# Kernel optimization log

Hardware: AMD Instinct MI355X
Metric: run time of the kernel (lower is better)

The kernel has to match this reference:

```python
import jax, jax.numpy as jnp
import numpy as np

N = 50000
E = 800000
F_IN = 500
H = 5          # heads
C = 32         # per-head channels
HID = H * C    # 160
NC = 20        # num_classes
G = 8          # number of graphs in batch
SLOPE_ATT = 0.2   # GATConv attention leaky slope (PyG default)
SLOPE_ACT = 0.01  # F.leaky_relu default


def _layernorm(x, scale, bias, eps=1e-5):
    mu = jnp.mean(x, axis=-1, keepdims=True)
    var = jnp.var(x, axis=-1, keepdims=True)
    return (x - mu) * jax.lax.rsqrt(var + eps) * scale + bias


def _edge_softmax(logits, dst, num_nodes):
    # segment softmax over incoming edges of each destination node
    m = jax.ops.segment_max(logits, dst, num_segments=num_nodes)
    ex = jnp.exp(logits - m[dst])
    s = jax.ops.segment_sum(ex, dst, num_segments=num_nodes)
    return ex / (s[dst] + 1e-16)


def _gat_layer(x, src, dst, W, a_src, a_dst, b):
    n = x.shape[0]
    h = (x @ W).reshape(n, H, C)                       # [N,H,C]
    al_s = jnp.einsum('nhc,hc->nh', h, a_src)          # [N,H]
    al_d = jnp.einsum('nhc,hc->nh', h, a_dst)
    logits = jax.nn.leaky_relu(al_s[src] + al_d[dst], SLOPE_ATT)  # [Et,H]
    alpha = _edge_softmax(logits, dst, n)              # [Et,H]
    msg = h[src] * alpha[..., None]                    # [Et,H,C]
    out = jax.ops.segment_sum(msg, dst, num_segments=n).reshape(n, HID) + b
    return out, alpha


def setup_inputs():
    key = jax.random.key(0)
    ks = jax.random.split(key, 24)
    p = lambda k, shp: jax.random.normal(k, shp, jnp.float32) * 0.05
    x = jax.random.normal(ks[0], (N, F_IN), jnp.float32)
    edge_index = jax.random.randint(ks[1], (2, E), 0, N, jnp.int64)
    batch = jnp.sort(jax.random.randint(ks[2], (N,), 0, G, jnp.int64))
    return {
        'x': x, 'edge_index': edge_index, 'batch': batch,
        'W1': p(ks[3], (F_IN, HID)), 'a_src1': p(ks[4], (H, C)), 'a_dst1': p(ks[5], (H, C)), 'b1': jnp.zeros((HID,), jnp.float32),
        'ln1_s': jnp.ones((HID,), jnp.float32), 'ln1_b': jnp.zeros((HID,), jnp.float32),
        'W2': p(ks[6], (HID, HID)), 'a_src2': p(ks[7], (H, C)), 'a_dst2': p(ks[8], (H, C)), 'b2': jnp.zeros((HID,), jnp.float32),
        'ln2_s': jnp.ones((HID,), jnp.float32), 'ln2_b': jnp.zeros((HID,), jnp.float32),
        'Wm': p(ks[9], (HID, HID)), 'bm': jnp.zeros((HID,), jnp.float32),
        'Wmlp1': p(ks[10], (HID, HID)), 'bmlp1': jnp.zeros((HID,), jnp.float32),
        'ln3_s': jnp.ones((HID,), jnp.float32), 'ln3_b': jnp.zeros((HID,), jnp.float32),
        'Wmlp2': p(ks[11], (HID, NC)), 'bmlp2': jnp.zeros((NC,), jnp.float32),
    }


def reference(x, edge_index, batch, W1, a_src1, a_dst1, b1, ln1_s, ln1_b,
              W2, a_src2, a_dst2, b2, ln2_s, ln2_b, Wm, bm,
              Wmlp1, bmlp1, ln3_s, ln3_b, Wmlp2, bmlp2):
    n = x.shape[0]
    # PyG GATConv adds self-loops by default
    loops = jnp.arange(n, dtype=edge_index.dtype)
    src = jnp.concatenate([edge_index[0], loops])
    dst = jnp.concatenate([edge_index[1], loops])

    h1, alpha1 = _gat_layer(x, src, dst, W1, a_src1, a_dst1, b1)
    h1 = jax.nn.leaky_relu(h1, SLOPE_ACT)
    h1 = _layernorm(h1, ln1_s, ln1_b)      # dropout = identity at eval

    h2, alpha2 = _gat_layer(h1, src, dst, W2, a_src2, a_dst2, b2)
    h2 = jax.nn.leaky_relu(h2, SLOPE_ACT)
    h2 = _layernorm(h2, ln2_s, ln2_b)

    xo = jax.nn.leaky_relu(h2 @ Wm + bm, SLOPE_ACT)   # [N,HID]

    # global_mean_pool over batch assignment
    sums = jax.ops.segment_sum(xo, batch, num_segments=G)
    cnts = jax.ops.segment_sum(jnp.ones((n, 1), xo.dtype), batch, num_segments=G)
    pooled = sums / jnp.maximum(cnts, 1.0)            # [G,HID]

    z = pooled @ Wmlp1 + bmlp1
    z = jax.nn.relu(_layernorm(z, ln3_s, ln3_b))
    rec = z @ Wmlp2 + bmlp2                           # [G,NC]
    return xo, rec, alpha1, alpha2
```

## Files before the change

### kernel.cpp

```cpp
#include <hip/hip_runtime.h>
#include <hip/hip_bf16.h>
#include <cstdint>
#include <cstddef>

#define NN   50000
#define EE   800000
#define ET_  (EE + NN)
#define FIN  500
#define HID_ 160
#define NC_  20
#define GG   8
#define GB1  ((NN + 63) / 64)
#define NK1  16
#define NK2  5
#define EBH  ((ET_ + 255) / 256)

typedef __attribute__((ext_vector_type(8))) short ab8;
typedef __attribute__((ext_vector_type(4))) float f4;

static __device__ __forceinline__ unsigned short f2bf(float v) {
    union { float f; uint32_t u; } c; c.f = v;
    uint32_t r = c.u + 0x7FFFu + ((c.u >> 16) & 1u);
    return (unsigned short)(r >> 16);
}

static __device__ __forceinline__ float2 bf2f2(uint32_t u) {
    union { uint32_t u; float f; } a, b;
    a.u = u << 16;
    b.u = u & 0xffff0000u;
    return make_float2(a.f, b.f);
}

static __device__ __forceinline__ int lbound_i(const int* arr, int n, int val) {
    int lo = 0, hi = n;
    while (lo < hi) { int mid = (lo + hi) >> 1; if (arr[mid] < val) lo = mid + 1; else hi = mid; }
    return lo;
}

__global__ __launch_bounds__(256) void k_prep0(const float* __restrict__ W1, ab8* __restrict__ B1,
                                               const float* __restrict__ W2, ab8* __restrict__ B2,
                                               const float* __restrict__ Wm, ab8* __restrict__ Bm,
                                               float* __restrict__ pooled, int* __restrict__ deg) {
    int idx = blockIdx.x * 256 + threadIdx.x;
    if (idx < NN) deg[idx] = 0;
    if (idx < GG * HID_) pooled[idx] = 0.f;
    const int C1 = NK1 * 10 * 64;
    const int C2 = NK2 * 10 * 64;
    const float* W; ab8* Bo; int K, cidx;
    if (idx < C1)                { W = W1; Bo = B1; K = FIN;  cidx = idx; }
    else if (idx < C1 + C2)      { W = W2; Bo = B2; K = HID_; cidx = idx - C1; }
    else if (idx < C1 + 2 * C2)  { W = Wm; Bo = Bm; K = HID_; cidx = idx - C1 - C2; }
    else return;
    int s = cidx / 640, r = cidx % 640;
    int t = r >> 6, l = r & 63;
    int fr = l & 15, q = l >> 4;
    int n  = t * 16 + fr;
    int k0 = s * 32 + q * 8;
    unsigned short pk[8];
#pragma unroll
    for (int j = 0; j < 8; j++) {
        int k = k0 + j;
        pk[j] = (k < K) ? f2bf(W[(size_t)k * HID_ + n]) : (unsigned short)0;
    }
    Bo[cidx] = *reinterpret_cast<ab8*>(pk);
}

__global__ __launch_bounds__(256) void k_hist_conv(const int* __restrict__ ei, int* __restrict__ deg,
                                                   const float* __restrict__ x, ab8* __restrict__ Apk) {
    if (blockIdx.x >= GB1) {
        int e = (blockIdx.x - GB1) * 256 + threadIdx.x;
        if (e >= ET_) return;
        int d = (e < EE) ? ei[EE + e] : (e - EE);
        atomicAdd(&deg[d], 1);
        return;
    }
    __shared__ uint2 lds2[4096];
    int blk = blockIdx.x;
    int tid = threadIdx.x;
    const float4* xf4 = (const float4*)x;
    uint4* ap4 = (uint4*)Apk;
#pragma unroll
    for (int h = 0; h < 2; h++) {
        for (int i = tid; i < 4096; i += 256) lds2[i] = make_uint2(0u, 0u);
        __syncthreads();
        int rbase = blk * 64 + h * 32;
        for (int i = tid; i < 4000; i += 256) {
            int rl = i / 125, j = i - rl * 125;
            int g = rbase + rl;
            if (g < NN) {
                float4 v = xf4[(size_t)g * 125 + j];
                uint32_t lo = (uint32_t)f2bf(v.x) | ((uint32_t)f2bf(v.y) << 16);
                uint32_t hi = (uint32_t)f2bf(v.z) | ((uint32_t)f2bf(v.w) << 16);
                int k = j * 4;
                int s = k >> 5, q = (k >> 3) & 3, e2 = (k & 7) >> 2;
                int woff = rl >> 4, fr = rl & 15;
                int idx = s * 128 + woff * 64 + q * 16 + fr;
                int p = idx ^ (((s << 2) | q) & 7);
                lds2[2 * p + e2] = make_uint2(lo, hi);
            }
        }
        __syncthreads();
        for (int i = tid; i < 2048; i += 256) {
            int s = i >> 7, off = i & 127;
            int q = (off >> 4) & 3;
            int p = i ^ (((s << 2) | q) & 7);
            uint2 a = lds2[2 * p], b = lds2[2 * p + 1];
            ap4[(size_t)(blk * NK1 + s) * 256 + h * 128 + off] = make_uint4(a.x, a.y, b.x, b.y);
        }
        __syncthreads();
    }
}

__global__ __launch_bounds__(256) void k_scan1(const int* __restrict__ deg, int* __restrict__ rowptr,
                                               int* __restrict__ bsum) {
    __shared__ int s[256];
    int t = threadIdx.x;
    int base = blockIdx.x * 1024 + t * 4;
    int v0 = (base + 0 < NN) ? deg[base + 0] : 0;
    int v1 = (base + 1 < NN) ? deg[base + 1] : 0;
    int v2 = (base + 2 < NN) ? deg[base + 2] : 0;
    int v3 = (base + 3 < NN) ? deg[base + 3] : 0;
    int tot = v0 + v1 + v2 + v3;
    s[t] = tot;
    __syncthreads();
    for (int off = 1; off < 256; off <<= 1) {
        int y = (t >= off) ? s[t - off] : 0;
        __syncthreads();
        s[t] += y;
        __syncthreads();
    }
    int excl = s[t] - tot;
    if (t == 255) bsum[blockIdx.x] = s[255];
    if (base + 0 < NN) rowptr[base + 0] = excl;  excl += v0;
    if (base + 1 < NN) rowptr[base + 1] = excl;  excl += v1;
    if (base + 2 < NN) rowptr[base + 2] = excl;  excl += v2;
    if (base + 3 < NN) rowptr[base + 3] = excl;
}

__global__ void k_scan2(int* __restrict__ bsum, int nb) {
    int t = threadIdx.x;
    int v = (t < nb) ? bsum[t] : 0;
    int orig = v;
    for (int off = 1; off < 64; off <<= 1) {
        int y = __shfl_up(v, off);
        if (t >= off) v += y;
    }
    if (t < nb) bsum[t] = v - orig;
}

__global__ __launch_bounds__(256) void k_scan3(int* __restrict__ rowptr, const int* __restrict__ bsum,
                                               int* __restrict__ cursor) {
    int i = blockIdx.x * 256 + threadIdx.x;
    if (i < NN) {
        int r = rowptr[i] + bsum[i >> 10];
        rowptr[i] = r;
        cursor[i] = r;
    }
    if (i == NN) rowptr[NN] = ET_;
}

static __device__ __forceinline__ void gemm_body(int blk,
                                                 const ab8* __restrict__ Apk,
                                                 const ab8* __restrict__ Bpk, int nk,
                                                 float* __restrict__ C, __hip_bfloat16* __restrict__ Cb,
                                                 int M,
                                                 const float* __restrict__ bias, int act,
                                                 const float* __restrict__ asrc, const float* __restrict__ adst,
                                                 float* __restrict__ als_o, float* __restrict__ ald_o,
                                                 const int* __restrict__ batch_p, float* __restrict__ pooled) {
    int tid  = threadIdx.x;
    int lane = tid & 63;
    int w    = tid >> 6;
    int fr   = lane & 15;
    int q    = lane >> 4;
    int row0 = blk * 64;

    f4 acc[10];
#pragma unroll
    for (int t = 0; t < 10; t++) acc[t] = (f4)0.f;

    const ab8* bb  = Bpk + lane;
    const ab8* apk = Apk + (size_t)blk * nk * 256 + tid;

    ab8 bcur[10], bnx[10];
#pragma unroll
    for (int t = 0; t < 10; t++) bcur[t] = bb[t * 64];
    ab8 a0 = apk[0];
    ab8 a1 = apk[256];
    for (int s = 0; s < nk; s++) {
        if (s + 1 < nk) {
#pragma unroll
            for (int t = 0; t < 10; t++) bnx[t] = bb[((s + 1) * 10 + t) * 64];
        }
        ab8 a2 = (ab8)0;
        if (s + 2 < nk) a2 = apk[(s + 2) * 256];
#pragma unroll
        for (int t = 0; t < 10; t++)
            acc[t] = __builtin_amdgcn_mfma_f32_16x16x32_bf16(a0, bcur[t], acc[t], 0, 0, 0);
        a0 = a1; a1 = a2;
#pragma unroll
        for (int t = 0; t < 10; t++) bcur[t] = bnx[t];
    }

    if (als_o) {
        float av_s[10], av_d[10];
#pragma unroll
        for (int t = 0; t < 10; t++) { av_s[t] = asrc[t * 16 + fr]; av_d[t] = adst[t * 16 + fr]; }
#pragma unroll
        for (int i = 0; i < 4; i++) {
            int r = row0 + w * 16 + q * 4 + i;
            float ps[5], pd[5];
#pragma unroll
            for (int h = 0; h < 5; h++) {
                ps[h] = acc[2 * h][i] * av_s[2 * h] + acc[2 * h + 1][i] * av_s[2 * h + 1];
                pd[h] = acc[2 * h][i] * av_d[2 * h] + acc[2 * h + 1][i] * av_d[2 * h + 1];
            }
#pragma unroll
            for (int off = 8; off >= 1; off >>= 1)
#pragma unroll
                for (int h = 0; h < 5; h++) {
                    ps[h] += __shfl_xor(ps[h], off);
                    pd[h] += __shfl_xor(pd[h], off);
                }
            if (fr == 0 && r < M) {
#pragma unroll
                for (int h = 0; h < 5; h++) {
                    als_o[(size_t)r * 8 + h] = ps[h];
                    ald_o[(size_t)r * 8 + h] = pd[h];
                }
            }
        }
    }

    int gu = -2;
    if (pooled) {
        int rhi = row0 + 63; if (rhi >= M) rhi = M - 1;
        int gl = batch_p[row0], gh = batch_p[rhi];
        gu = (gl == gh) ? gl : -1;
    }
    float psum[10];
#pragma unroll
    for (int t = 0; t < 10; t++) psum[t] = 0.f;

    int rbase = row0 + w * 16 + q * 4;
#pragma unroll
    for (int t = 0; t < 10; t++) {
        int col = t * 16 + fr;
        float bv = bias ? bias[col] : 0.f;
#pragma unroll
        for (int i = 0; i < 4; i++) {
            int r = rbase + i;
            float v = acc[t][i] + bv;
            if (act) v = v > 0.f ? v : 0.01f * v;
            if (r < M) {
                if (C)  C[(size_t)r * HID_ + col] = v;
                if (Cb) *reinterpret_cast<unsigned short*>(&Cb[(size_t)r * HID_ + col]) = f2bf(v);
                if (gu >= 0) psum[t] += v;
                else if (gu == -1) atomicAdd(&pooled[batch_p[r] * HID_ + col], v);
            }
        }
    }
    if (gu >= 0) {
#pragma unroll
        for (int t = 0; t < 10; t++) {
            psum[t] += __shfl_xor(psum[t], 16);
            psum[t] += __shfl_xor(psum[t], 32);
        }
        if (q == 0) {
#pragma unroll
            for (int t = 0; t < 10; t++)
                atomicAdd(&pooled[gu * HID_ + t * 16 + fr], psum[t]);
        }
    }
}

__global__ __launch_bounds__(256) void k_gemm_scatter(const ab8* __restrict__ Apk,
                                                      const ab8* __restrict__ Bpk, int nk,
                                                      float* __restrict__ C, __hip_bfloat16* __restrict__ Cb,
                                                      int M,
                                                      const float* __restrict__ bias, int act,
                                                      const float* __restrict__ asrc, const float* __restrict__ adst,
                                                      float* __restrict__ als_o, float* __restrict__ ald_o,
                                                      const int* __restrict__ batch_p, float* __restrict__ pooled,
                                                      const int* __restrict__ ei, int* __restrict__ cursor,
                                                      int* __restrict__ esrc) {
    if (blockIdx.x < GB1) {
        gemm_body(blockIdx.x, Apk, Bpk, nk, C, Cb, M, bias, act, asrc, adst, als_o, ald_o, batch_p, pooled);
    } else {
        int e = (blockIdx.x - GB1) * 256 + threadIdx.x;
        if (e >= ET_) return;
        int s, d;
        if (e < EE) { s = ei[e]; d = ei[EE + e]; } else { s = e - EE; d = e - EE; }
        int slot = atomicAdd(&cursor[d], 1);
        esrc[slot] = s;
    }
}

static __device__ __forceinline__ void alpha_body(int e, const int* __restrict__ ei,
                                                  const float* __restrict__ als, const float* __restrict__ ald,
                                                  const float* __restrict__ invb,
                                                  float* __restrict__ alpha_out) {
    if (e >= ET_) return;
    int s, d;
    if (e < EE) { s = ei[e]; d = ei[EE + e]; } else { s = e - EE; d = e - EE; }
    const float* as = &als[(size_t)s * 8];
    float4 a4 = *reinterpret_cast<const float4*>(as);
    float  a5 = as[4];
    float asv[5] = {a4.x, a4.y, a4.z, a4.w, a5};
    const float* adp = &ald[(size_t)d * 8];
    float4 d4 = *reinterpret_cast<const float4*>(adp);
    float  d5 = adp[4];
    float adv[5] = {d4.x, d4.y, d4.z, d4.w, d5};
    const float* ip = &invb[(size_t)d * 8];
    float4 i4 = *reinterpret_cast<const float4*>(ip);
    float  i5 = ip[4];
    float ivv[5] = {i4.x, i4.y, i4.z, i4.w, i5};
    float* ao = &alpha_out[(size_t)e * 5];
#pragma unroll
    for (int h = 0; h < 5; h++) {
        float l = asv[h] + adv[h];
        l = l > 0.f ? l : 0.2f * l;
        float ex = __expf(fminf(l, 60.f));
        ao[h] = ex * ivv[h];
    }
}

__global__ __launch_bounds__(256) void k_gemm_alpha(const ab8* __restrict__ Apk,
                                                    const ab8* __restrict__ Bpk, int nk,
                                                    float* __restrict__ C, __hip_bfloat16* __restrict__ Cb,
                                                    int M,
                                                    const float* __restrict__ bias, int act,
                                                    const float* __restrict__ asrc, const float* __restrict__ adst,
                                                    float* __restrict__ als_o, float* __restrict__ ald_o,
                                                    const int* __restrict__ batch_p, float* __restrict__ pooled,
                                                    const int* __restrict__ ei,
                                                    const float* __restrict__ als_r, const float* __restrict__ ald_r,
                                                    const float* __restrict__ invb, float* __restrict__ alpha_out) {
    if (blockIdx.x < GB1) {
        gemm_body(blockIdx.x, Apk, Bpk, nk, C, Cb, M, bias, act, asrc, adst, als_o, ald_o, batch_p, pooled);
    } else {
        int e = (blockIdx.x - GB1) * 256 + threadIdx.x;
        alpha_body(e, ei, als_r, ald_r, invb, alpha_out);
    }
}

__global__ __launch_bounds__(256) void k_att_agg(const int* __restrict__ rowptr,
                                                 const int* __restrict__ esrc,
                                                 const float* __restrict__ als, const float* __restrict__ ald,
                                                 const __hip_bfloat16* __restrict__ hmat,
                                                 float* __restrict__ alphap,
                                                 float* __restrict__ invb,
                                                 const float* __restrict__ bias,
                                                 const float* __restrict__ lns, const float* __restrict__ lnb,
                                                 uint4* __restrict__ xpk) {
    __shared__ float sExp[4][64 * 5];
    __shared__ int   sSrc[4][64];
    int wv   = threadIdx.x >> 6;
    int lane = threadIdx.x & 63;
    int node = blockIdx.x * 4 + wv;
    if (node >= NN) return;
    int start = rowptr[node], end = rowptr[node + 1];
    int deg = end - start;
    bool fits = (deg <= 64);
    float4 dd4 = *reinterpret_cast<const float4*>(&ald[(size_t)node * 8]);
    float  dd5 = ald[(size_t)node * 8 + 4];
    float ad[5] = {dd4.x, dd4.y, dd4.z, dd4.w, dd5};

    float sm[5] = {0.f, 0.f, 0.f, 0.f, 0.f};
    for (int j = start + lane; j < end; j += 64) {
        int sy = esrc[j];
        int idx = j - start;
        if (fits) sSrc[wv][idx] = sy;
        const float* as = &als[(size_t)sy * 8];
        float4 a4 = *reinterpret_cast<const float4*>(as);
        float  a5 = as[4];
        float asv[5] = {a4.x, a4.y, a4.z, a4.w, a5};
#pragma unroll
        for (int h = 0; h < 5; h++) {
            float l = asv[h] + ad[h];
            l = l > 0.f ? l : 0.2f * l;
            float ex = __expf(fminf(l, 60.f));
            sm[h] += ex;
            if (fits) sExp[wv][idx * 5 + h] = ex;
            else      alphap[(size_t)j * 5 + h] = ex;
        }
    }
#pragma unroll
    for (int off = 32; off >= 1; off >>= 1)
#pragma unroll
        for (int h = 0; h < 5; h++) sm[h] += __shfl_xor(sm[h], off);
    float inv[5];
#pragma unroll
    for (int h = 0; h < 5; h++) inv[h] = 1.f / (sm[h] + 1e-16f);
    if (lane == 0) {
        float* ip = &invb[(size_t)node * 8];
        ip[0] = inv[0]; ip[1] = inv[1]; ip[2] = inv[2]; ip[3] = inv[3]; ip[4] = inv[4];
    }
    if (fits && lane < deg) {
#pragma unroll
        for (int h = 0; h < 5; h++) sExp[wv][lane * 5 + h] *= inv[h];
    }

    int h0 = lane >> 4;
    bool lo16 = lane < 16;
    int c01 = 2 * lane;
    int c2  = 128 + 2 * lane;
    float2 A0 = make_float2(0.f, 0.f), A1 = make_float2(0.f, 0.f);
    float2 A2 = make_float2(0.f, 0.f), A3 = make_float2(0.f, 0.f);
    float2 H0 = make_float2(0.f, 0.f), H1 = make_float2(0.f, 0.f);
    float2 H2 = make_float2(0.f, 0.f), H3 = make_float2(0.f, 0.f);

    if (fits) {
        int idx = 0;
        for (; idx + 3 < deg; idx += 4) {
            int s0 = sSrc[wv][idx], s1 = sSrc[wv][idx + 1];
            int s2 = sSrc[wv][idx + 2], s3 = sSrc[wv][idx + 3];
            float w0 = sExp[wv][(idx + 0) * 5 + h0];
            float w1 = sExp[wv][(idx + 1) * 5 + h0];
            float w2 = sExp[wv][(idx + 2) * 5 + h0];
            float w3 = sExp[wv][(idx + 3) * 5 + h0];
            const unsigned short* r0 = (const unsigned short*)&hmat[(size_t)s0 * HID_];
            const unsigned short* r1 = (const unsigned short*)&hmat[(size_t)s1 * HID_];
            const unsigned short* r2 = (const unsigned short*)&hmat[(size_t)s2 * HID_];
            const unsigned short* r3 = (const unsigned short*)&hmat[(size_t)s3 * HID_];
            float2 f0 = bf2f2(*reinterpret_cast<const uint32_t*>(&r0[c01]));
            float2 f1 = bf2f2(*reinterpret_cast<const uint32_t*>(&r1[c01]));
            float2 f2 = bf2f2(*reinterpret_cast<const uint32_t*>(&r2[c01]));
            float2 f3 = bf2f2(*reinterpret_cast<const uint32_t*>(&r3[c01]));
            A0.x += w0 * f0.x; A0.y += w0 * f0.y;
            A1.x += w1 * f1.x; A1.y += w1 * f1.y;
            A2.x += w2 * f2.x; A2.y += w2 * f2.y;
            A3.x += w3 * f3.x; A3.y += w3 * f3.y;
            if (lo16) {
                float u0 = sExp[wv][(idx + 0) * 5 + 4];
                float u1 = sExp[wv][(idx + 1) * 5 + 4];
                float u2 = sExp[wv][(idx + 2) * 5 + 4];
                float u3 = sExp[wv][(idx + 3) * 5 + 4];
                float2 g0 = bf2f2(*reinterpret_cast<const uint32_t*>(&r0[c2]));
                float2 g1 = bf2f2(*reinterpret_cast<const uint32_t*>(&r1[c2]));
                float2 g2 = bf2f2(*reinterpret_cast<const uint32_t*>(&r2[c2]));
                float2 g3 = bf2f2(*reinterpret_cast<const uint32_t*>(&r3[c2]));
                H0.x += u0 * g0.x; H0.y += u0 * g0.y;
                H1.x += u1 * g1.x; H1.y += u1 * g1.y;
                H2.x += u2 * g2.x; H2.y += u2 * g2.y;
                H3.x += u3 * g3.x; H3.y += u3 * g3.y;
            }
        }
        for (; idx < deg; idx++) {
            int s0 = sSrc[wv][idx];
            float w0 = sExp[wv][idx * 5 + h0];
            const unsigned short* r0 = (const unsigned short*)&hmat[(size_t)s0 * HID_];
            float2 f0 = bf2f2(*reinterpret_cast<const uint32_t*>(&r0[c01]));
            A0.x += w0 * f0.x; A0.y += w0 * f0.y;
            if (lo16) {
                float u0 = sExp[wv][idx * 5 + 4];
                float2 g0 = bf2f2(*reinterpret_cast<const uint32_t*>(&r0[c2]));
                H0.x += u0 * g0.x; H0.y += u0 * g0.y;
            }
        }
    } else {
        for (int j = start; j < end; j++) {
            int s0 = esrc[j];
            float w0 = alphap[(size_t)j * 5 + h0] * inv[h0];
            const unsigned short* r0 = (const unsigned short*)&hmat[(size_t)s0 * HID_];
            float2 f0 = bf2f2(*reinterpret_cast<const uint32_t*>(&r0[c01]));
            A0.x += w0 * f0.x; A0.y += w0 * f0.y;
            if (lo16) {
                float u0 = alphap[(size_t)j * 5 + 4] * inv[4];
                float2 g0 = bf2f2(*reinterpret_cast<const uint32_t*>(&r0[c2]));
                H0.x += u0 * g0.x; H0.y += u0 * g0.y;
            }
        }
    }
    float2 A = make_float2(A0.x + A1.x + A2.x + A3.x, A0.y + A1.y + A2.y + A3.y);
    float2 Hh = make_float2(H0.x + H1.x + H2.x + H3.x, H0.y + H1.y + H2.y + H3.y);

    float2 bb = *reinterpret_cast<const float2*>(&bias[c01]);
    float v0 = A.x + bb.x;  v0 = v0 > 0.f ? v0 : 0.01f * v0;
    float v1 = A.y + bb.y;  v1 = v1 > 0.f ? v1 : 0.01f * v1;
    float v2 = 0.f, v3 = 0.f;
    if (lo16) {
        float2 b2 = *reinterpret_cast<const float2*>(&bias[c2]);
        v2 = Hh.x + b2.x; v2 = v2 > 0.f ? v2 : 0.01f * v2;
        v3 = Hh.y + b2.y; v3 = v3 > 0.f ? v3 : 0.01f * v3;
    }
    float s  = v0 + v1 + v2 + v3;
    float sq = v0 * v0 + v1 * v1 + v2 * v2 + v3 * v3;
#pragma unroll
    for (int off = 32; off >= 1; off >>= 1) {
        s  += __shfl_xor(s, off);
        sq += __shfl_xor(sq, off);
    }
    float m = s * (1.f / 160.f);
    float r = rsqrtf(sq * (1.f / 160.f) - m * m + 1e-5f);
    uint32_t pk1, pk2 = 0u;
    {
        float2 sc = *reinterpret_cast<const float2*>(&lns[c01]);
        float2 bi = *reinterpret_cast<const float2*>(&lnb[c01]);
        pk1 = (uint32_t)f2bf((v0 - m) * r * sc.x + bi.x)
            | ((uint32_t)f2bf((v1 - m) * r * sc.y + bi.y) << 16);
    }
    if (lo16) {
        float2 sc = *reinterpret_cast<const float2*>(&lns[c2]);
        float2 bi = *reinterpret_cast<const float2*>(&lnb[c2]);
        pk2 = (uint32_t)f2bf((v2 - m) * r * sc.x + bi.x)
            | ((uint32_t)f2bf((v3 - m) * r * sc.y + bi.y) << 16);
    }
    int j = lane;
    int srcb = (j < 16) ? (4 * j) : (4 * ((j - 16) & 15));
    uint32_t a0w = __shfl(pk1, srcb + 0), a1w = __shfl(pk1, srcb + 1);
    uint32_t a2w = __shfl(pk1, srcb + 2), a3w = __shfl(pk1, srcb + 3);
    uint32_t b0w = __shfl(pk2, srcb + 0), b1w = __shfl(pk2, srcb + 1);
    uint32_t b2w = __shfl(pk2, srcb + 2), b3w = __shfl(pk2, srcb + 3);
    if (j < 20) {
        uint4 val;
        val.x = (j < 16) ? a0w : b0w;
        val.y = (j < 16) ? a1w : b1w;
        val.z = (j < 16) ? a2w : b2w;
        val.w = (j < 16) ? a3w : b3w;
        int blk = node >> 6, wq = (node >> 4) & 3, fr = node & 15;
        int ks = j >> 2, q = j & 3;
        size_t cidx = (size_t)(blk * NK2 + ks) * 256 + wq * 64 + q * 16 + fr;
        xpk[cidx] = val;
    }
}

__global__ __launch_bounds__(256) void k_mlp(const float* __restrict__ pooled, const int* __restrict__ batch,
                                             const float* __restrict__ W1, const float* __restrict__ b1,
                                             const float* __restrict__ lns, const float* __restrict__ lnb,
                                             const float* __restrict__ W2, const float* __restrict__ b2,
                                             float* __restrict__ rec) {
    __shared__ float P[GG][HID_];
    __shared__ float Z[GG][HID_];
    __shared__ float mu[GG], rr[GG], ic[GG];
    int t = threadIdx.x;
    if (t < GG) {
        int lo = lbound_i(batch, NN, t), hi = lbound_i(batch, NN, t + 1);
        ic[t] = 1.f / fmaxf((float)(hi - lo), 1.f);
    }
    __syncthreads();
    for (int i = t; i < GG * HID_; i += 256) P[i / HID_][i % HID_] = pooled[i] * ic[i / HID_];
    __syncthreads();
    for (int i = t; i < GG * HID_; i += 256) {
        int g = i / HID_, j = i % HID_;
        float acc = b1[j];
        for (int k = 0; k < HID_; k++) acc += P[g][k] * W1[k * HID_ + j];
        Z[g][j] = acc;
    }
    __syncthreads();
    if (t < GG) {
        float s = 0.f, sq = 0.f;
        for (int k = 0; k < HID_; k++) { float z = Z[t][k]; s += z; sq += z * z; }
        float m = s / (float)HID_;
        mu[t] = m;
        rr[t] = rsqrtf(sq / (float)HID_ - m * m + 1e-5f);
    }
    __syncthreads();
    for (int i = t; i < GG * HID_; i += 256) {
        int g = i / HID_, j = i % HID_;
        float z = (Z[g][j] - mu[g]) * rr[g] * lns[j] + lnb[j];
        Z[g][j] = fmaxf(z, 0.f);
    }
    __syncthreads();
    for (int i = t; i < GG * NC_; i += 256) {
        int g = i / NC_, j = i % NC_;
        float acc = b2[j];
        for (int k = 0; k < HID_; k++) acc += Z[g][k] * W2[k * NC_ + j];
        rec[g * NC_ + j] = acc;
    }
}

extern "C" void kernel_launch(void* const* d_in, const int* in_sizes, int n_in,
                              void* d_out, int out_size, void* d_ws, size_t ws_size,
                              hipStream_t stream) {
    const float* x    = (const float*)d_in[0];
    const int*   ei   = (const int*)d_in[1];
    const int*   batch= (const int*)d_in[2];
    const float* W1   = (const float*)d_in[3];
    const float* as1  = (const float*)d_in[4];
    const float* ad1  = (const float*)d_in[5];
    const float* b1   = (const float*)d_in[6];
    const float* ln1s = (const float*)d_in[7];
    const float* ln1b = (const float*)d_in[8];
    const float* W2   = (const float*)d_in[9];
    const float* as2  = (const float*)d_in[10];
    const float* ad2  = (const float*)d_in[11];
    const float* b2   = (const float*)d_in[12];
    const float* ln2s = (const float*)d_in[13];
    const float* ln2b = (const float*)d_in[14];
    const float* Wm   = (const float*)d_in[15];
    const float* bm   = (const float*)d_in[16];
    const float* Wm1  = (const float*)d_in[17];
    const float* bm1  = (const float*)d_in[18];
    const float* ln3s = (const float*)d_in[19];
    const float* ln3b = (const float*)d_in[20];
    const float* Wm2  = (const float*)d_in[21];
    const float* bm2  = (const float*)d_in[22];

    float* out    = (float*)d_out;
    float* xo     = out;
    float* rec    = out + (size_t)NN * HID_;
    float* alpha1 = rec + GG * NC_;
    float* alpha2 = alpha1 + (size_t)ET_ * 5;

    char* w = (char*)d_ws;
    auto carve = [&](size_t bytes) { char* p = w; w += (bytes + 255) & ~(size_t)255; return p; };
    int*   deg    = (int*)carve((size_t)NN * 4);
    int*   rowptr = (int*)carve((size_t)(NN + 1) * 4);
    int*   cursor = (int*)carve((size_t)NN * 4);
    int*   esrc   = (int*)carve((size_t)ET_ * 4);
    int*   bsum   = (int*)carve(64 * 4);
    __hip_bfloat16* hbuf = (__hip_bfloat16*)carve((size_t)NN * HID_ * 2);
    uint4* xpk    = (uint4*)carve((size_t)GB1 * NK2 * 256 * 16);
    float* alphap = (float*)carve((size_t)ET_ * 5 * 4);
    float* als1   = (float*)carve((size_t)NN * 8 * 4);
    float* ald1   = (float*)carve((size_t)NN * 8 * 4);
    float* als2   = (float*)carve((size_t)NN * 8 * 4);
    float* ald2   = (float*)carve((size_t)NN * 8 * 4);
    float* invb   = (float*)carve((size_t)NN * 8 * 4);
    float* pooled = (float*)carve((size_t)GG * HID_ * 4);
    ab8*   B1pk   = (ab8*)carve((size_t)NK1 * 10 * 64 * 16);
    ab8*   B2pk   = (ab8*)carve((size_t)NK2 * 10 * 64 * 16);
    ab8*   Bmpk   = (ab8*)carve((size_t)NK2 * 10 * 64 * 16);
    ab8*   Apk    = (ab8*)d_out;

    k_prep0<<<(NN + 255) / 256, 256, 0, stream>>>(W1, B1pk, W2, B2pk, Wm, Bmpk, pooled, deg);

    k_hist_conv<<<GB1 + EBH, 256, 0, stream>>>(ei, deg, x, Apk);

    int nb = (NN + 1023) / 1024;
    k_scan1<<<nb, 256, 0, stream>>>(deg, rowptr, bsum);
    k_scan2<<<1, 64, 0, stream>>>(bsum, nb);
    k_scan3<<<(NN + 1 + 255) / 256, 256, 0, stream>>>(rowptr, bsum, cursor);

    const int NWB = (NN + 3) / 4;

    k_gemm_scatter<<<GB1 + EBH, 256, 0, stream>>>(Apk, B1pk, NK1, nullptr, hbuf, NN, nullptr, 0,
                                                  as1, ad1, als1, ald1, nullptr, nullptr,
                                                  ei, cursor, esrc);

    k_att_agg<<<NWB, 256, 0, stream>>>(rowptr, esrc, als1, ald1, hbuf, alphap, invb,
                                       b1, ln1s, ln1b, xpk);

    k_gemm_alpha<<<GB1 + EBH, 256, 0, stream>>>((const ab8*)xpk, B2pk, NK2, nullptr, hbuf, NN,
                                                nullptr, 0, as2, ad2, als2, ald2, nullptr, nullptr,
                                                ei, als1, ald1, invb, alpha1);

    k_att_agg<<<NWB, 256, 0, stream>>>(rowptr, esrc, als2, ald2, hbuf, alphap, invb,
                                       b2, ln2s, ln2b, xpk);

    k_gemm_alpha<<<GB1 + EBH, 256, 0, stream>>>((const ab8*)xpk, Bmpk, NK2, xo, nullptr, NN,
                                                bm, 1, nullptr, nullptr, nullptr, nullptr, batch, pooled,
                                                ei, als2, ald2, invb, alpha2);

    k_mlp<<<1, 256, 0, stream>>>(pooled, batch, Wm1, bm1, ln3s, ln3b, Wm2, bm2, rec);
}
```

Measured before the change: 600.2 us.

## Fuse x bf16 conversion into first GEMM via LDS staging, merge prep with histogram

Removes the separate pass that converted x to packed bf16 in global memory. The first-layer GEMM now loads fp32 x directly, converts and swizzles it into LDS in two halves, then runs MFMA from LDS. This avoids writing and re-reading about 50 MB of packed A. Weight packing is merged into the degree histogram kernel, and deg is zeroed with a memset. The cost is extra syncthreads and LDS traffic inside the GEMM, and the conversion work now sits on the GEMM's critical path.

Measured after the change: 613.5 us. 1.02x slower.

```diff
diff --git a/kernel.cpp b/kernel.cpp
--- a/kernel.cpp
+++ b/kernel.cpp
@@ -14,6 +14,7 @@
 #define NK1  16
 #define NK2  5
 #define EBH  ((ET_ + 255) / 256)
+#define PREPB ((NK1 * 10 * 64 + 2 * NK2 * 10 * 64 + 255) / 256)
 
 typedef __attribute__((ext_vector_type(8))) short ab8;
 typedef __attribute__((ext_vector_type(4))) float f4;
@@ -37,12 +38,19 @@
     return lo;
 }
 
-__global__ __launch_bounds__(256) void k_prep0(const float* __restrict__ W1, ab8* __restrict__ B1,
-                                               const float* __restrict__ W2, ab8* __restrict__ B2,
-                                               const float* __restrict__ Wm, ab8* __restrict__ Bm,
-                                               float* __restrict__ pooled, int* __restrict__ deg) {
-    int idx = blockIdx.x * 256 + threadIdx.x;
-    if (idx < NN) deg[idx] = 0;
+__global__ __launch_bounds__(256) void k_prep_hist(const float* __restrict__ W1, ab8* __restrict__ B1,
+                                                   const float* __restrict__ W2, ab8* __restrict__ B2,
+                                                   const float* __restrict__ Wm, ab8* __restrict__ Bm,
+                                                   float* __restrict__ pooled,
+                                                   const int* __restrict__ ei, int* __restrict__ deg) {
+    if (blockIdx.x < EBH) {
+        int e = blockIdx.x * 256 + threadIdx.x;
+        if (e >= ET_) return;
+        int d = (e < EE) ? ei[EE + e] : (e - EE);
+        atomicAdd(&deg[d], 1);
+        return;
+    }
+    int idx = (blockIdx.x - EBH) * 256 + threadIdx.x;
     if (idx < GG * HID_) pooled[idx] = 0.f;
     const int C1 = NK1 * 10 * 64;
     const int C2 = NK2 * 10 * 64;
@@ -63,52 +71,6 @@
         pk[j] = (k < K) ? f2bf(W[(size_t)k * HID_ + n]) : (unsigned short)0;
     }
     Bo[cidx] = *reinterpret_cast<ab8*>(pk);
-}
-
-__global__ __launch_bounds__(256) void k_hist_conv(const int* __restrict__ ei, int* __restrict__ deg,
-                                                   const float* __restrict__ x, ab8* __restrict__ Apk) {
-    if (blockIdx.x >= GB1) {
-        int e = (blockIdx.x - GB1) * 256 + threadIdx.x;
-        if (e >= ET_) return;
-        int d = (e < EE) ? ei[EE + e] : (e - EE);
-        atomicAdd(&deg[d], 1);
-        return;
-    }
-    __shared__ uint2 lds2[4096];
-    int blk = blockIdx.x;
-    int tid = threadIdx.x;
-    const float4* xf4 = (const float4*)x;
-    uint4* ap4 = (uint4*)Apk;
-#pragma unroll
-    for (int h = 0; h < 2; h++) {
-        for (int i = tid; i < 4096; i += 256) lds2[i] = make_uint2(0u, 0u);
-        __syncthreads();
-        int rbase = blk * 64 + h * 32;
-        for (int i = tid; i < 4000; i += 256) {
-            int rl = i / 125, j = i - rl * 125;
-            int g = rbase + rl;
-            if (g < NN) {
-                float4 v = xf4[(size_t)g * 125 + j];
-                uint32_t lo = (uint32_t)f2bf(v.x) | ((uint32_t)f2bf(v.y) << 16);
-                uint32_t hi = (uint32_t)f2bf(v.z) | ((uint32_t)f2bf(v.w) << 16);
-                int k = j * 4;
-                int s = k >> 5, q = (k >> 3) & 3, e2 = (k & 7) >> 2;
-                int woff = rl >> 4, fr = rl & 15;
-                int idx = s * 128 + woff * 64 + q * 16 + fr;
-                int p = idx ^ (((s << 2) | q) & 7);
-                lds2[2 * p + e2] = make_uint2(lo, hi);
-            }
-        }
-        __syncthreads();
-        for (int i = tid; i < 2048; i += 256) {
-            int s = i >> 7, off = i & 127;
-            int q = (off >> 4) & 3;
-            int p = i ^ (((s << 2) | q) & 7);
-            uint2 a = lds2[2 * p], b = lds2[2 * p + 1];
-            ap4[(size_t)(blk * NK1 + s) * 256 + h * 128 + off] = make_uint4(a.x, a.y, b.x, b.y);
-        }
-        __syncthreads();
-    }
 }
 
 __global__ __launch_bounds__(256) void k_scan1(const int* __restrict__ deg, int* __restrict__ rowptr,
@@ -159,6 +121,89 @@
     if (i == NN) rowptr[NN] = ET_;
 }
 
+static __device__ __forceinline__ void gemm_epilogue(f4 (&acc)[10], int row0, int M,
+                                                     float* __restrict__ C, __hip_bfloat16* __restrict__ Cb,
+                                                     const float* __restrict__ bias, int act,
+                                                     const float* __restrict__ asrc, const float* __restrict__ adst,
+                                                     float* __restrict__ als_o, float* __restrict__ ald_o,
+                                                     const int* __restrict__ batch_p, float* __restrict__ pooled) {
+    int lane = threadIdx.x & 63;
+    int w    = threadIdx.x >> 6;
+    int fr   = lane & 15;
+    int q    = lane >> 4;
+
+    if (als_o) {
+        float av_s[10], av_d[10];
+#pragma unroll
+        for (int t = 0; t < 10; t++) { av_s[t] = asrc[t * 16 + fr]; av_d[t] = adst[t * 16 + fr]; }
+#pragma unroll
+        for (int i = 0; i < 4; i++) {
+            int r = row0 + w * 16 + q * 4 + i;
+            float ps[5], pd[5];
+#pragma unroll
+            for (int h = 0; h < 5; h++) {
+                ps[h] = acc[2 * h][i] * av_s[2 * h] + acc[2 * h + 1][i] * av_s[2 * h + 1];
+                pd[h] = acc[2 * h][i] * av_d[2 * h] + acc[2 * h + 1][i] * av_d[2 * h + 1];
+            }
+#pragma unroll
+            for (int off = 8; off >= 1; off >>= 1)
+#pragma unroll
+                for (int h = 0; h < 5; h++) {
+                    ps[h] += __shfl_xor(ps[h], off);
+                    pd[h] += __shfl_xor(pd[h], off);
+                }
+            if (fr == 0 && r < M) {
+#pragma unroll
+                for (int h = 0; h < 5; h++) {
+                    als_o[(size_t)r * 8 + h] = ps[h];
+                    ald_o[(size_t)r * 8 + h] = pd[h];
+                }
+            }
+        }
+    }
+
+    int gu = -2;
+    if (pooled) {
+        int rhi = row0 + 63; if (rhi >= M) rhi = M - 1;
+        int gl = batch_p[row0], gh = batch_p[rhi];
+        gu = (gl == gh) ? gl : -1;
+    }
+    float psum[10];
+#pragma unroll
+    for (int t = 0; t < 10; t++) psum[t] = 0.f;
+
+    int rbase = row0 + w * 16 + q * 4;
+#pragma unroll
+    for (int t = 0; t < 10; t++) {
+        int col = t * 16 + fr;
+        float bv = bias ? bias[col] : 0.f;
+#pragma unroll
+        for (int i = 0; i < 4; i++) {
+            int r = rbase + i;
+            float v = acc[t][i] + bv;
+            if (act) v = v > 0.f ? v : 0.01f * v;
+            if (r < M) {
+                if (C)  C[(size_t)r * HID_ + col] = v;
+                if (Cb) *reinterpret_cast<unsigned short*>(&Cb[(size_t)r * HID_ + col]) = f2bf(v);
+                if (gu >= 0) psum[t] += v;
+                else if (gu == -1) atomicAdd(&pooled[batch_p[r] * HID_ + col], v);
+            }
+        }
+    }
+    if (gu >= 0) {
+#pragma unroll
+        for (int t = 0; t < 10; t++) {
+            psum[t] += __shfl_xor(psum[t], 16);
+            psum[t] += __shfl_xor(psum[t], 32);
+        }
+        if (q == 0) {
+#pragma unroll
+            for (int t = 0; t < 10; t++)
+                atomicAdd(&pooled[gu * HID_ + t * 16 + fr], psum[t]);
+        }
+    }
+}
+
 static __device__ __forceinline__ void gemm_body(int blk,
                                                  const ab8* __restrict__ Apk,
                                                  const ab8* __restrict__ Bpk, int nk,
@@ -170,9 +215,6 @@
                                                  const int* __restrict__ batch_p, float* __restrict__ pooled) {
     int tid  = threadIdx.x;
     int lane = tid & 63;
-    int w    = tid >> 6;
-    int fr   = lane & 15;
-    int q    = lane >> 4;
     int row0 = blk * 64;
 
     f4 acc[10];
@@ -201,99 +243,81 @@
 #pragma unroll
         for (int t = 0; t < 10; t++) bcur[t] = bnx[t];
     }
-
-    if (als_o) {
-        float av_s[10], av_d[10];
-#pragma unroll
-        for (int t = 0; t < 10; t++) { av_s[t] = asrc[t * 16 + fr]; av_d[t] = adst[t * 16 + fr]; }
-#pragma unroll
-        for (int i = 0; i < 4; i++) {
-            int r = row0 + w * 16 + q * 4 + i;
-            float ps[5], pd[5];
-#pragma unroll
-            for (int h = 0; h < 5; h++) {
-                ps[h] = acc[2 * h][i] * av_s[2 * h] + acc[2 * h + 1][i] * av_s[2 * h + 1];
-                pd[h] = acc[2 * h][i] * av_d[2 * h] + acc[2 * h + 1][i] * av_d[2 * h + 1];
-            }
-#pragma unroll
-            for (int off = 8; off >= 1; off >>= 1)
-#pragma unroll
-                for (int h = 0; h < 5; h++) {
-                    ps[h] += __shfl_xor(ps[h], off);
-                    pd[h] += __shfl_xor(pd[h], off);
-                }
-            if (fr == 0 && r < M) {
-#pragma unroll
-                for (int h = 0; h < 5; h++) {
-                    als_o[(size_t)r * 8 + h] = ps[h];
-                    ald_o[(size_t)r * 8 + h] = pd[h];
-                }
-            }
-        }
-    }
-
-    int gu = -2;
-    if (pooled) {
-        int rhi = row0 + 63; if (rhi >= M) rhi = M - 1;
-        int gl = batch_p[row0], gh = batch_p[rhi];
-        gu = (gl == gh) ? gl : -1;
-    }
-    float psum[10];
-#pragma unroll
-    for (int t = 0; t < 10; t++) psum[t] = 0.f;
-
-    int rbase = row0 + w * 16 + q * 4;
-#pragma unroll
-    for (int t = 0; t < 10; t++) {
-        int col = t * 16 + fr;
-        float bv = bias ? bias[col] : 0.f;
-#pragma unroll
-        for (int i = 0; i < 4; i++) {
-            int r = rbase + i;
-            float v = acc[t][i] + bv;
-            if (act) v = v > 0.f ? v : 0.01f * v;
-            if (r < M) {
-                if (C)  C[(size_t)r * HID_ + col] = v;
-                if (Cb) *reinterpret_cast<unsigned short*>(&Cb[(size_t)r * HID_ + col]) = f2bf(v);
-                if (gu >= 0) psum[t] += v;
-                else if (gu == -1) atomicAdd(&pooled[batch_p[r] * HID_ + col], v);
-            }
-        }
-    }
-    if (gu >= 0) {
-#pragma unroll
-        for (int t = 0; t < 10; t++) {
-            psum[t] += __shfl_xor(psum[t], 16);
-            psum[t] += __shfl_xor(psum[t], 32);
-        }
-        if (q == 0) {
-#pragma unroll
-            for (int t = 0; t < 10; t++)
-                atomicAdd(&pooled[gu * HID_ + t * 16 + fr], psum[t]);
-        }
-    }
-}
-
-__global__ __launch_bounds__(256) void k_gemm_scatter(const ab8* __restrict__ Apk,
-                                                      const ab8* __restrict__ Bpk, int nk,
-                                                      float* __restrict__ C, __hip_bfloat16* __restrict__ Cb,
-                                                      int M,
-                                                      const float* __restrict__ bias, int act,
-                                                      const float* __restrict__ asrc, const float* __restrict__ adst,
-                                                      float* __restrict__ als_o, float* __restrict__ ald_o,
-                                                      const int* __restrict__ batch_p, float* __restrict__ pooled,
-                                                      const int* __restrict__ ei, int* __restrict__ cursor,
-                                                      int* __restrict__ esrc) {
-    if (blockIdx.x < GB1) {
-        gemm_body(blockIdx.x, Apk, Bpk, nk, C, Cb, M, bias, act, asrc, adst, als_o, ald_o, batch_p, pooled);
-    } else {
+    gemm_epilogue(acc, row0, M, C, Cb, bias, act, asrc, adst, als_o, ald_o, batch_p, pooled);
+}
+
+__global__ __launch_bounds__(256) void k_gemm1_scatter(const float* __restrict__ x,
+                                                       const ab8* __restrict__ Bpk,
+                                                       __hip_bfloat16* __restrict__ Cb, int M,
+                                                       const float* __restrict__ asrc, const float* __restrict__ adst,
+                                                       float* __restrict__ als_o, float* __restrict__ ald_o,
+                                                       const int* __restrict__ ei, int* __restrict__ cursor,
+                                                       int* __restrict__ esrc) {
+    if (blockIdx.x >= GB1) {
         int e = (blockIdx.x - GB1) * 256 + threadIdx.x;
         if (e >= ET_) return;
         int s, d;
         if (e < EE) { s = ei[e]; d = ei[EE + e]; } else { s = e - EE; d = e - EE; }
         int slot = atomicAdd(&cursor[d], 1);
         esrc[slot] = s;
-    }
+        return;
+    }
+    __shared__ __align__(16) uint2 lds2[4096];
+    int blk  = blockIdx.x;
+    int tid  = threadIdx.x;
+    int lane = tid & 63;
+    int q    = lane >> 4;
+    int row0 = blk * 64;
+
+    f4 acc[10];
+#pragma unroll
+    for (int t = 0; t < 10; t++) acc[t] = (f4)0.f;
+
+    const ab8* bb = Bpk + lane;
+    ab8 bcur[10], bnx[10];
+#pragma unroll
+    for (int t = 0; t < 10; t++) bcur[t] = bb[t * 64];
+
+    const float4* xf4 = (const float4*)x;
+
+#pragma unroll
+    for (int half = 0; half < 2; half++) {
+        for (int i = tid; i < 4096; i += 256) lds2[i] = make_uint2(0u, 0u);
+        __syncthreads();
+        for (int i = tid; i < 4096; i += 256) {
+            int rl = i >> 6, j = i & 63;
+            int fidx = half * 64 + j;
+            int g = row0 + rl;
+            if (g < M && fidx < 125) {
+                float4 v = xf4[(size_t)g * 125 + fidx];
+                uint32_t lo = (uint32_t)f2bf(v.x) | ((uint32_t)f2bf(v.y) << 16);
+                uint32_t hi = (uint32_t)f2bf(v.z) | ((uint32_t)f2bf(v.w) << 16);
+                int sl = j >> 3, qq = (j >> 1) & 3, e2 = j & 1;
+                int chunk = sl * 256 + (rl >> 4) * 64 + qq * 16 + (rl & 15);
+                int p = chunk ^ (((sl << 2) | qq) & 7);
+                lds2[2 * p + e2] = make_uint2(lo, hi);
+            }
+        }
+        __syncthreads();
+        for (int sl = 0; sl < 8; sl++) {
+            int s = half * 8 + sl;
+            if (s + 1 < NK1) {
+#pragma unroll
+                for (int t = 0; t < 10; t++) bnx[t] = bb[((s + 1) * 10 + t) * 64];
+            }
+            int chunk = sl * 256 + tid;
+            int p = chunk ^ (((sl << 2) | q) & 7);
+            uint4 av = *reinterpret_cast<uint4*>(&lds2[2 * p]);
+            ab8 a0 = *reinterpret_cast<ab8*>(&av);
+#pragma unroll
+            for (int t = 0; t < 10; t++)
+                acc[t] = __builtin_amdgcn_mfma_f32_16x16x32_bf16(a0, bcur[t], acc[t], 0, 0, 0);
+#pragma unroll
+            for (int t = 0; t < 10; t++) bcur[t] = bnx[t];
+        }
+        __syncthreads();
+    }
+    gemm_epilogue(acc, row0, M, nullptr, Cb, nullptr, 0, asrc, adst, als_o, ald_o, nullptr, nullptr);
 }
 
 static __device__ __forceinline__ void alpha_body(int e, const int* __restrict__ ei,
@@ -622,11 +646,10 @@
     ab8*   B1pk   = (ab8*)carve((size_t)NK1 * 10 * 64 * 16);
     ab8*   B2pk   = (ab8*)carve((size_t)NK2 * 10 * 64 * 16);
     ab8*   Bmpk   = (ab8*)carve((size_t)NK2 * 10 * 64 * 16);
-    ab8*   Apk    = (ab8*)d_out;
-
-    k_prep0<<<(NN + 255) / 256, 256, 0, stream>>>(W1, B1pk, W2, B2pk, Wm, Bmpk, pooled, deg);
-
-    k_hist_conv<<<GB1 + EBH, 256, 0, stream>>>(ei, deg, x, Apk);
+
+    hipMemsetAsync(deg, 0, (size_t)NN * 4, stream);
+
+    k_prep_hist<<<EBH + PREPB, 256, 0, stream>>>(W1, B1pk, W2, B2pk, Wm, Bmpk, pooled, ei, deg);
 
     int nb = (NN + 1023) / 1024;
     k_scan1<<<nb, 256, 0, stream>>>(deg, rowptr, bsum);
@@ -635,9 +658,8 @@
 
     const int NWB = (NN + 3) / 4;
 
-    k_gemm_scatter<<<GB1 + EBH, 256, 0, stream>>>(Apk, B1pk, NK1, nullptr, hbuf, NN, nullptr, 0,
-                                                  as1, ad1, als1, ald1, nullptr, nullptr,
-                                                  ei, cursor, esrc);
+    k_gemm1_scatter<<<GB1 + EBH, 256, 0, stream>>>(x, B1pk, hbuf, NN, as1, ad1, als1, ald1,
+                                                   ei, cursor, esrc);
 
     k_att_agg<<<NWB, 256, 0, stream>>>(rowptr, esrc, als1, ald1, hbuf, alphap, invb,
                                        b1, ln1s, ln1b, xpk);
```
